# Kernel tuning notes

Hardware: AMD Instinct MI355X
Metric: run time of the kernel (lower is better)

## Reference

```python
import jax, jax.numpy as jnp
import numpy as np

D_MODEL = 1024
N_HEADS = 16
HEAD_DIM = D_MODEL // N_HEADS


def setup_inputs() -> dict:
    key = jax.random.key(0)
    k1, k2, k3, k4, k5 = jax.random.split(key, 5)
    s = 0.02
    return {
        "x": jax.random.normal(k1, (2, 2048, D_MODEL), dtype=jnp.float32),
        "w_qkv": jax.random.normal(k2, (D_MODEL, 3 * D_MODEL), dtype=jnp.float32) * s,
        "b_qkv": jax.random.normal(k3, (3 * D_MODEL,), dtype=jnp.float32) * s,
        "w_proj": jax.random.normal(k4, (D_MODEL, D_MODEL), dtype=jnp.float32) * s,
        "b_proj": jax.random.normal(k5, (D_MODEL,), dtype=jnp.float32) * s,
    }


def reference(x, w_qkv, b_qkv, w_proj, b_proj):
    B, T, C = x.shape
    # fused qkv projection: [B,T,3C] -> [3,B,H,T,Dh]
    qkv = x @ w_qkv + b_qkv
    qkv = qkv.reshape(B, T, 3, N_HEADS, HEAD_DIM).transpose(2, 0, 3, 1, 4)
    q, k, v = qkv[0], qkv[1], qkv[2]
    scale = 1.0 / np.sqrt(HEAD_DIM).astype(np.float32)
    att = jnp.einsum("bhtd,bhsd->bhts", q, k) * scale  # [B,H,T,T]
    causal = jnp.triu(jnp.ones((T, T), dtype=bool), k=1)
    att = jnp.where(causal, -jnp.inf, att)
    att = jax.nn.softmax(att, axis=-1)
    # dropout is identity in eval / p=0
    out = jnp.einsum("bhts,bhsd->bhtd", att, v)  # [B,H,T,Dh]
    out = out.transpose(0, 2, 1, 3).reshape(B, T, C)
    return out @ w_proj + b_proj
```

## Files before the change

kernel.cpp:

```cpp
#include <hip/hip_runtime.h>
#include <hip/hip_bf16.h>
#include <stdint.h>

#define MROWS 4096
#define DMODEL 1024
#define NQKV 3072
#define TSEQ 2048

typedef __attribute__((ext_vector_type(8))) short short8;
typedef __attribute__((ext_vector_type(4))) short short4v;
typedef __attribute__((ext_vector_type(4))) float floatx4;
typedef unsigned short ushort_t;

#define TILE_ELEMS 4608
#define BH_TILE_STRIDE 147456

#define QSCALE 0.1803368801111204f

static __device__ __forceinline__ unsigned short f2bf(float f) {
    union { float f; unsigned u; } v; v.f = f;
    unsigned r = v.u + 0x7fff + ((v.u >> 16) & 1);
    return (unsigned short)(r >> 16);
}


static __device__ __forceinline__ floatx4 mfma16(short4v a, short4v b, floatx4 c) {
#if defined(__HIP_DEVICE_COMPILE__)
#if __has_builtin(__builtin_amdgcn_mfma_f32_16x16x16bf16_1k)
    return __builtin_amdgcn_mfma_f32_16x16x16bf16_1k(a, b, c, 0, 0, 0);
#else
#error "mfma 16x16x16 bf16 builtin unavailable on device"
#endif
#else
    return c;
#endif
}

static __device__ __forceinline__ unsigned pk2bf(float a, float b) {
    unsigned ua = __float_as_uint(a) + 0x8000u;
    unsigned ub = __float_as_uint(b) + 0x8000u;
#if defined(__HIP_DEVICE_COMPILE__) && __has_builtin(__builtin_amdgcn_perm)
    return __builtin_amdgcn_perm(ub, ua, 0x07060302u);
#else
    return (ua >> 16) | (ub & 0xFFFF0000u);
#endif
}

static __device__ __forceinline__ unsigned cvtpk(float a, float b) {
#if defined(__HIP_DEVICE_COMPILE__)
    unsigned r;
    asm("v_cvt_pk_bf16_f32 %0, %1, %2" : "=v"(r) : "v"(a), "v"(b));
    return r;
#else
    return pk2bf(a, b);
#endif
}

static __device__ __forceinline__ float exp2_fast(float x) {
#if defined(__HIP_DEVICE_COMPILE__) && __has_builtin(__builtin_amdgcn_exp2f)
    return __builtin_amdgcn_exp2f(x);
#else
    return exp2f(x);
#endif
}

static __device__ __forceinline__ void glds16(const void* g, void* l) {
    __builtin_amdgcn_global_load_lds(
        (const __attribute__((address_space(1))) void*)g,
        (__attribute__((address_space(3))) void*)l, 16, 0, 0);
}

__global__ void cast_f32_bf16(const float* __restrict__ in,
                              ushort_t* __restrict__ out, int n) {
    int i = (blockIdx.x * blockDim.x + threadIdx.x) * 4;
    if (i < n) {
        float4 f = *(const float4*)(in + i);
        ushort4 o;
        o.x = f2bf(f.x); o.y = f2bf(f.y); o.z = f2bf(f.z); o.w = f2bf(f.w);
        *(ushort4*)(out + i) = o;
    }
}

__global__ void transpose_cast(const float* __restrict__ in,
                               ushort_t* __restrict__ out, int R, int C) {
    __shared__ float tile[32][33];
    int c0 = blockIdx.x * 32, r0 = blockIdx.y * 32;
    int tx = threadIdx.x & 31, ty = threadIdx.x >> 5;
    for (int i = 0; i < 4; i++) {
        int r = ty + i * 8;
        tile[r][tx] = in[(size_t)(r0 + r) * C + c0 + tx];
    }
    __syncthreads();
    for (int i = 0; i < 4; i++) {
        int r = ty + i * 8;
        out[(size_t)(c0 + r) * R + r0 + tx] = f2bf(tile[tx][r]);
    }
}

__global__ void transpose_v(const ushort_t* __restrict__ in,
                            ushort_t* __restrict__ out) {
    __shared__ ushort_t T[64][72];
    int tile = blockIdx.x, bh = blockIdx.y;
    int tid = threadIdx.x;
    int row = tid >> 2, q4 = tid & 3;
    const ushort_t* ip = in + ((size_t)bh * TSEQ + tile * 64) * 64;
#pragma unroll
    for (int p = 0; p < 2; p++) {
        int c = q4 * 16 + p * 8;
        *(uint4*)(&T[row][c]) = *(const uint4*)(ip + (size_t)row * 64 + c);
    }
    __syncthreads();
    ushort_t* op = out + (size_t)bh * BH_TILE_STRIDE + (size_t)tile * TILE_ELEMS;
#pragma unroll
    for (int p = 0; p < 2; p++) {
        int cbase = q4 * 16 + p * 8;
        ushort_t tmp[8];
#pragma unroll
        for (int e = 0; e < 8; e++) {
            int cp = cbase + e;
            int Q = cp >> 4, SB = (cp >> 2) & 3, J = cp & 3;
            int s = SB * 16 + Q * 4 + J;
            tmp[e] = T[s][row];
        }
        *(uint4*)(op + (size_t)row * 72 + cbase) = *(uint4*)tmp;
    }
}

template <int EPI, int MFRAG, int PERXCD>
__global__ __launch_bounds__(256, 3)
void gemm_glds(const ushort_t* __restrict__ A,
               const ushort_t* __restrict__ Bt,
               const float* __restrict__ bias,
               void* __restrict__ out0, void* __restrict__ out1, void* __restrict__ out2,
               int M, int N, int K) {
    __shared__ ushort_t As[2][MFRAG * 32 * 32];
    __shared__ ushort_t Bs[2][128 * 32];
    int tid = threadIdx.x;
    int wave = tid >> 6, lane = tid & 63;
    int quad = lane >> 4, l16 = lane & 15;
    int id = blockIdx.x;
    int xcd = id & 7, sidx = id >> 3;
    int m_idx = xcd * PERXCD + (sidx & (PERXCD - 1));
    int n_idx = sidx / PERXCD;
    int m0 = m_idx * (MFRAG * 32), n0 = n_idx * 128;
    int wm = (wave & 1) * (MFRAG * 16), wn = (wave >> 1) * 64;

    const floatx4 zero = {0.f, 0.f, 0.f, 0.f};
    floatx4 acc[MFRAG][4];
#pragma unroll
    for (int i = 0; i < MFRAG; i++)
#pragma unroll
        for (int j = 0; j < 4; j++) acc[i][j] = zero;

    int srow = tid >> 2, sc = tid & 3;
    const ushort_t* ag = A  + (size_t)(m0 + srow) * K + sc * 8;
    const ushort_t* bg = Bt + (size_t)(n0 + srow) * K + sc * 8;
    int woff = wave * 512;

    glds16(ag, &As[0][woff]);
    if (MFRAG == 4) glds16(ag + (size_t)64 * K, &As[0][woff + 2048]);
    glds16(bg, &Bs[0][woff]);
    glds16(bg + (size_t)64 * K, &Bs[0][woff + 2048]);
    __syncthreads();

    int cur = 0;
    for (int k0 = 0; k0 < K; k0 += 32) {
        if (k0 + 32 < K) {
            int nb = cur ^ 1, kn = k0 + 32;
            glds16(ag + kn, &As[nb][woff]);
            if (MFRAG == 4) glds16(ag + (size_t)64 * K + kn, &As[nb][woff + 2048]);
            glds16(bg + kn, &Bs[nb][woff]);
            glds16(bg + (size_t)64 * K + kn, &Bs[nb][woff + 2048]);
        }
        short8 af[MFRAG], bf[4];
#pragma unroll
        for (int i = 0; i < MFRAG; i++)
            af[i] = *(const short8*)(&As[cur][(wm + i * 16 + l16) * 32 + quad * 8]);
#pragma unroll
        for (int j = 0; j < 4; j++)
            bf[j] = *(const short8*)(&Bs[cur][(wn + j * 16 + l16) * 32 + quad * 8]);
#pragma unroll
        for (int i = 0; i < MFRAG; i++)
#pragma unroll
            for (int j = 0; j < 4; j++)
                acc[i][j] = __builtin_amdgcn_mfma_f32_16x16x32_bf16(
                    af[i], bf[j], acc[i][j], 0, 0, 0);
        __syncthreads();
        cur ^= 1;
    }

    int sec = n0 >> 10;
    ushort_t* dst = (ushort_t*)(sec == 0 ? out0 : (sec == 1 ? out1 : out2));

    if (EPI == 1 && sec == 2) {
#pragma unroll
        for (int i = 0; i < MFRAG; i++) {
            int row = m0 + wm + i * 16 + quad * 4;
            int Abits = ((wm >> 4) + i) & 3;
            int b = row >> 11, t = row & 2047;
            int tile = t >> 6;
            int colp = 16 * quad + 4 * Abits;
#pragma unroll
            for (int j = 0; j < 4; j++) {
                int col = n0 + wn + j * 16 + l16;
                int within = col & 1023, h = within >> 6, d = within & 63;
                size_t bh = (size_t)(b * 16 + h);
                float bvs = bias[col];
                ushort4 o;
                o.x = f2bf(acc[i][j][0] + bvs);
                o.y = f2bf(acc[i][j][1] + bvs);
                o.z = f2bf(acc[i][j][2] + bvs);
                o.w = f2bf(acc[i][j][3] + bvs);
                *(ushort4*)(dst + bh * BH_TILE_STRIDE + (size_t)tile * TILE_ELEMS
                            + (size_t)d * 72 + colp) = o;
            }
        }
        return;
    }

#pragma unroll
    for (int i = 0; i < MFRAG; i++) {
        int row = m0 + wm + i * 16 + quad * 4;
#pragma unroll
        for (int j = 0; j < 4; j++) {
            int col = n0 + wn + j * 16 + l16;
            float bvs = bias[col];
#pragma unroll
            for (int r = 0; r < 4; r++) {
                float v = acc[i][j][r] + bvs;
                int rowr = row + r;
                if (EPI == 0) {
                    ((float*)out0)[(size_t)rowr * N + col] = v;
                } else {
                    int b = rowr >> 11, t = rowr & 2047;
                    int within = col & 1023, h = within >> 6, d = within & 63;
                    size_t bh = (size_t)(b * 16 + h);
                    if (sec == 0)
                        dst[(bh * 2048 + t) * 64 + d] = f2bf(v * QSCALE);
                    else if (sec == 1)
                        dst[bh * BH_TILE_STRIDE + (size_t)(t >> 6) * TILE_ELEMS
                            + (size_t)(t & 63) * 72 + d] = f2bf(v);
                    else
                        dst[(bh * 2048 + t) * 64 + d] = f2bf(v);
                }
            }
        }
    }
}

__global__ __launch_bounds__(128, 2)
void attn_split(const ushort_t* __restrict__ Qb,
                const ushort_t* __restrict__ Kt,
                const ushort_t* __restrict__ Vt,
                ushort_t* __restrict__ outb,
                float* __restrict__ PO_a, float* __restrict__ PO_b,
                float* __restrict__ Pl_a, float* __restrict__ Pl_b) {
    __shared__ ushort_t Ks[2][64 * 72];
    __shared__ ushort_t Vs[2][64 * 72];
    int tid = threadIdx.x;
    int wave = tid >> 6, lane = tid & 63;
    int quad = lane >> 4, l16 = lane & 15;
    int id = blockIdx.x;
    int g = id >> 3;
    int bh = (id & 7) * 4 + (g >> 5);
    int rem = g & 31;
    int p = rem >> 1, sub = rem & 1;
    int b = bh >> 4, h = bh & 15;
    const ushort_t* qh = Qb + (size_t)bh * TSEQ * 64;
    const ushort_t* kh = Kt + (size_t)bh * BH_TILE_STRIDE;
    const ushort_t* vh = Vt + (size_t)bh * BH_TILE_STRIDE;
    const floatx4 zero = {0.f, 0.f, 0.f, 0.f};
    const short4v ones = {(short)0x3F80, (short)0x3F80, (short)0x3F80, (short)0x3F80};
    int lo8 = lane * 8;

    int nseg = sub ? 1 : 2;
    for (int seg = 0; seg < nseg; seg++) {
        int qt, k0, cnt, mode;
        if (sub)           { qt = 31 - p; k0 = 16 - p; cnt = 16;     mode = 2; }
        else if (seg == 0) { qt = p;      k0 = 0;      cnt = p + 1;  mode = 0; }
        else               { qt = 31 - p; k0 = 0;      cnt = 16 - p; mode = 1; }

        short8 qf0[2], qf1[2];
#pragma unroll
        for (int qs = 0; qs < 2; qs++) {
            int qrow = qt * 64 + wave * 32 + qs * 16 + l16;
            qf0[qs] = *(const short8*)(qh + (size_t)qrow * 64 + quad * 8);
            qf1[qs] = *(const short8*)(qh + (size_t)qrow * 64 + 32 + quad * 8);
        }

        floatx4 Oacc[2][4];
#pragma unroll
        for (int qs = 0; qs < 2; qs++)
#pragma unroll
            for (int j = 0; j < 4; j++) Oacc[qs][j] = zero;
        floatx4 lacc[2];
        lacc[0] = zero; lacc[1] = zero;

        __syncthreads();
        {
            const ushort_t* kt0 = kh + (size_t)k0 * TILE_ELEMS;
            const ushort_t* vt0 = vh + (size_t)k0 * TILE_ELEMS;
#pragma unroll
            for (int c = 0; c < 5; c++) {
                int cc = wave + 2 * c;
                if (cc < 9) {
                    glds16(kt0 + cc * 512 + lo8, &Ks[0][cc * 512]);
                    glds16(vt0 + cc * 512 + lo8, &Vs[0][cc * 512]);
                }
            }
        }

        for (int step = 0; step < cnt; step++) {
            int cur = step & 1;
            __syncthreads();
            if (step + 1 < cnt) {
                const ushort_t* kt = kh + (size_t)(k0 + step + 1) * TILE_ELEMS;
                const ushort_t* vt = vh + (size_t)(k0 + step + 1) * TILE_ELEMS;
#pragma unroll
                for (int c = 0; c < 5; c++) {
                    int cc = wave + 2 * c;
                    if (cc < 9) {
                        glds16(kt + cc * 512 + lo8, &Ks[cur ^ 1][cc * 512]);
                        glds16(vt + cc * 512 + lo8, &Vs[cur ^ 1][cc * 512]);
                    }
                }
            }
            const ushort_t* ks = &Ks[cur][0];
            const ushort_t* vs = &Vs[cur][0];

            floatx4 S[2][4];
            __builtin_amdgcn_s_setprio(1);
#pragma unroll
            for (int sb = 0; sb < 4; sb++) {
                short8 kf0 = *(const short8*)(ks + (sb * 16 + l16) * 72 + quad * 8);
                short8 kf1 = *(const short8*)(ks + (sb * 16 + l16) * 72 + 32 + quad * 8);
#pragma unroll
                for (int qs = 0; qs < 2; qs++) {
                    floatx4 s = zero;
                    s = __builtin_amdgcn_mfma_f32_16x16x32_bf16(kf0, qf0[qs], s, 0, 0, 0);
                    s = __builtin_amdgcn_mfma_f32_16x16x32_bf16(kf1, qf1[qs], s, 0, 0, 0);
                    S[qs][sb] = s;
                }
            }
            __builtin_amdgcn_s_setprio(0);
            if (k0 + step == qt) {
#pragma unroll
                for (int qs = 0; qs < 2; qs++) {
                    int ql = wave * 32 + qs * 16 + l16;
#pragma unroll
                    for (int sb = 0; sb < 4; sb++)
#pragma unroll
                        for (int r = 0; r < 4; r++)
                            if (sb * 16 + quad * 4 + r > ql) S[qs][sb][r] = -1e30f;
                }
            }
#pragma unroll
            for (int qs = 0; qs < 2; qs++)
#pragma unroll
                for (int sb = 0; sb < 4; sb++)
#pragma unroll
                    for (int r = 0; r < 4; r++)
                        S[qs][sb][r] = exp2_fast(S[qs][sb][r]);

            short4v pf[2][4];
#pragma unroll
            for (int qs = 0; qs < 2; qs++)
#pragma unroll
                for (int sb = 0; sb < 4; sb++) {
                    union { unsigned u[2]; short4v v; } pk;
                    pk.u[0] = cvtpk(S[qs][sb][0], S[qs][sb][1]);
                    pk.u[1] = cvtpk(S[qs][sb][2], S[qs][sb][3]);
                    pf[qs][sb] = pk.v;
                }
            __builtin_amdgcn_s_setprio(1);
#pragma unroll
            for (int qs = 0; qs < 2; qs++) {
                lacc[qs] = mfma16(ones, pf[qs][0], lacc[qs]);
                lacc[qs] = mfma16(ones, pf[qs][1], lacc[qs]);
                lacc[qs] = mfma16(ones, pf[qs][2], lacc[qs]);
                lacc[qs] = mfma16(ones, pf[qs][3], lacc[qs]);
            }
#pragma unroll
            for (int jd = 0; jd < 4; jd++) {
                const ushort_t* vrow = vs + (jd * 16 + l16) * 72 + quad * 16;
                short8 vA = *(const short8*)(vrow);
                short8 vB = *(const short8*)(vrow + 8);
                short4v v0 = __builtin_shufflevector(vA, vA, 0, 1, 2, 3);
                short4v v1 = __builtin_shufflevector(vA, vA, 4, 5, 6, 7);
                short4v v2 = __builtin_shufflevector(vB, vB, 0, 1, 2, 3);
                short4v v3 = __builtin_shufflevector(vB, vB, 4, 5, 6, 7);
#pragma unroll
                for (int qs = 0; qs < 2; qs++) {
                    Oacc[qs][jd] = mfma16(v0, pf[qs][0], Oacc[qs][jd]);
                    Oacc[qs][jd] = mfma16(v1, pf[qs][1], Oacc[qs][jd]);
                    Oacc[qs][jd] = mfma16(v2, pf[qs][2], Oacc[qs][jd]);
                    Oacc[qs][jd] = mfma16(v3, pf[qs][3], Oacc[qs][jd]);
                }
            }
            __builtin_amdgcn_s_setprio(0);
        }

        if (mode == 0) {
#pragma unroll
            for (int qs = 0; qs < 2; qs++) {
                float rl = 1.0f / lacc[qs][0];
                int row = b * TSEQ + qt * 64 + wave * 32 + qs * 16 + l16;
#pragma unroll
                for (int jd = 0; jd < 4; jd++) {
                    int col = h * 64 + jd * 16 + quad * 4;
                    ushort4 o;
                    o.x = f2bf(Oacc[qs][jd][0] * rl);
                    o.y = f2bf(Oacc[qs][jd][1] * rl);
                    o.z = f2bf(Oacc[qs][jd][2] * rl);
                    o.w = f2bf(Oacc[qs][jd][3] * rl);
                    *(ushort4*)(outb + (size_t)row * DMODEL + col) = o;
                }
            }
        } else {
            float* PO = (mode == 1) ? PO_a : PO_b;
            float* Pl = (mode == 1) ? Pl_a : Pl_b;
#pragma unroll
            for (int qs = 0; qs < 2; qs++) {
                int prow = (qt - 16) * 64 + wave * 32 + qs * 16 + l16;
                size_t rbase = ((size_t)bh * 1024 + prow) * 64;
#pragma unroll
                for (int jd = 0; jd < 4; jd++)
                    *(floatx4*)(PO + rbase + jd * 16 + quad * 4) = Oacc[qs][jd];
                if (quad == 0) Pl[(size_t)bh * 1024 + prow] = lacc[qs][0];
            }
        }
    }
}

__global__ void attn_combine(const float* __restrict__ PO_a,
                             const float* __restrict__ PO_b,
                             const float* __restrict__ Pl_a,
                             const float* __restrict__ Pl_b,
                             ushort_t* __restrict__ outb) {
    int i = blockIdx.x * 256 + threadIdx.x;
    int row = i >> 4;
    int c4 = (i & 15) * 4;
    float rl = 1.0f / (Pl_a[row] + Pl_b[row]);
    floatx4 a = *(const floatx4*)(PO_a + (size_t)row * 64 + c4);
    floatx4 c = *(const floatx4*)(PO_b + (size_t)row * 64 + c4);
    int bh = row >> 10, prow = row & 1023;
    int b = bh >> 4, h = bh & 15;
    int orow = b * TSEQ + 1024 + prow;
    ushort4 o;
    o.x = f2bf((a[0] + c[0]) * rl);
    o.y = f2bf((a[1] + c[1]) * rl);
    o.z = f2bf((a[2] + c[2]) * rl);
    o.w = f2bf((a[3] + c[3]) * rl);
    *(ushort4*)(outb + (size_t)orow * DMODEL + h * 64 + c4) = o;
}

__global__ __launch_bounds__(256, 1)
void attn_paired(const ushort_t* __restrict__ Qb,
                 const ushort_t* __restrict__ Kt,
                 const ushort_t* __restrict__ Vt,
                 ushort_t* __restrict__ outb) {
    __shared__ ushort_t Ks[2][64 * 72];
    __shared__ ushort_t Vs[2][64 * 72];
    int tid = threadIdx.x;
    int wave = tid >> 6, lane = tid & 63;
    int quad = lane >> 4, l16 = lane & 15;
    int pair = blockIdx.x;
    int bh = blockIdx.y;
    int b = bh >> 4, h = bh & 15;
    const ushort_t* qh = Qb + (size_t)bh * TSEQ * 64;
    const ushort_t* kh = Kt + (size_t)bh * BH_TILE_STRIDE;
    const ushort_t* vh = Vt + (size_t)bh * BH_TILE_STRIDE;
    const floatx4 zero = {0.f, 0.f, 0.f, 0.f};
    int lo8 = lane * 8;

    for (int half = 0; half < 2; half++) {
        int qt = half ? (31 - pair) : pair;
        int q0 = qt * 64;
        int nsteps = qt + 1;

        int qrow = q0 + wave * 16 + l16;
        short8 qf0 = *(const short8*)(qh + (size_t)qrow * 64 + quad * 8);
        short8 qf1 = *(const short8*)(qh + (size_t)qrow * 64 + 32 + quad * 8);

        floatx4 Oacc[4];
#pragma unroll
        for (int j = 0; j < 4; j++) Oacc[j] = zero;
        float lsum = 0.f;

#pragma unroll
        for (int c = 0; c < 3; c++) {
            int cc = wave + 4 * c;
            if (cc < 9) {
                glds16(kh + cc * 512 + lo8, &Ks[0][cc * 512]);
                glds16(vh + cc * 512 + lo8, &Vs[0][cc * 512]);
            }
        }

        for (int step = 0; step < nsteps; step++) {
            int cur = step & 1;
            __syncthreads();
            if (step + 1 < nsteps) {
                const ushort_t* kt = kh + (size_t)(step + 1) * TILE_ELEMS;
                const ushort_t* vt = vh + (size_t)(step + 1) * TILE_ELEMS;
#pragma unroll
                for (int c = 0; c < 3; c++) {
                    int cc = wave + 4 * c;
                    if (cc < 9) {
                        glds16(kt + cc * 512 + lo8, &Ks[cur ^ 1][cc * 512]);
                        glds16(vt + cc * 512 + lo8, &Vs[cur ^ 1][cc * 512]);
                    }
                }
            }
            const ushort_t* ks = &Ks[cur][0];
            const ushort_t* vs = &Vs[cur][0];

            floatx4 S[4];
#pragma unroll
            for (int sb = 0; sb < 4; sb++) {
                short8 kf0 = *(const short8*)(ks + (sb * 16 + l16) * 72 + quad * 8);
                short8 kf1 = *(const short8*)(ks + (sb * 16 + l16) * 72 + 32 + quad * 8);
                floatx4 s = zero;
                s = __builtin_amdgcn_mfma_f32_16x16x32_bf16(kf0, qf0, s, 0, 0, 0);
                s = __builtin_amdgcn_mfma_f32_16x16x32_bf16(kf1, qf1, s, 0, 0, 0);
                S[sb] = s;
            }
            if (step == nsteps - 1) {
                int ql = wave * 16 + l16;
#pragma unroll
                for (int sb = 0; sb < 4; sb++)
#pragma unroll
                    for (int r = 0; r < 4; r++)
                        if (sb * 16 + quad * 4 + r > ql) S[sb][r] = -1e30f;
            }
            float sum = 0.f;
#pragma unroll
            for (int sb = 0; sb < 4; sb++)
#pragma unroll
                for (int r = 0; r < 4; r++) {
                    float p = exp2_fast(S[sb][r]);
                    S[sb][r] = p;
                    sum += p;
                }
            lsum += sum;

            short4v pf[4];
#pragma unroll
            for (int sb = 0; sb < 4; sb++) {
                union { unsigned u[2]; short4v v; } pk;
                pk.u[0] = pk2bf(S[sb][0], S[sb][1]);
                pk.u[1] = pk2bf(S[sb][2], S[sb][3]);
                pf[sb] = pk.v;
            }
#pragma unroll
            for (int jd = 0; jd < 4; jd++) {
                const ushort_t* vrow = vs + (jd * 16 + l16) * 72 + quad * 16;
                short8 vA = *(const short8*)(vrow);
                short8 vB = *(const short8*)(vrow + 8);
                short4v v0 = __builtin_shufflevector(vA, vA, 0, 1, 2, 3);
                short4v v1 = __builtin_shufflevector(vA, vA, 4, 5, 6, 7);
                short4v v2 = __builtin_shufflevector(vB, vB, 0, 1, 2, 3);
                short4v v3 = __builtin_shufflevector(vB, vB, 4, 5, 6, 7);
                Oacc[jd] = mfma16(v0, pf[0], Oacc[jd]);
                Oacc[jd] = mfma16(v1, pf[1], Oacc[jd]);
                Oacc[jd] = mfma16(v2, pf[2], Oacc[jd]);
                Oacc[jd] = mfma16(v3, pf[3], Oacc[jd]);
            }
        }
        {
            float l = lsum;
            l += __shfl_xor(l, 16);
            l += __shfl_xor(l, 32);
            float rl = 1.0f / l;
            int row = b * TSEQ + q0 + wave * 16 + l16;
#pragma unroll
            for (int jd = 0; jd < 4; jd++) {
                int col = h * 64 + jd * 16 + quad * 4;
                ushort4 o;
                o.x = f2bf(Oacc[jd][0] * rl);
                o.y = f2bf(Oacc[jd][1] * rl);
                o.z = f2bf(Oacc[jd][2] * rl);
                o.w = f2bf(Oacc[jd][3] * rl);
                *(ushort4*)(outb + (size_t)row * DMODEL + col) = o;
            }
        }
        __syncthreads();
    }
}

extern "C" void kernel_launch(void* const* d_in, const int* in_sizes, int n_in,
                              void* d_out, int out_size, void* d_ws, size_t ws_size,
                              hipStream_t stream) {
    const float* x      = (const float*)d_in[0];
    const float* w_qkv  = (const float*)d_in[1];
    const float* b_qkv  = (const float*)d_in[2];
    const float* w_proj = (const float*)d_in[3];
    const float* b_proj = (const float*)d_in[4];
    float* out = (float*)d_out;
    char* ws = (char*)d_ws;

    ushort_t* xb     = (ushort_t*)(ws);
    ushort_t* wqkvT  = (ushort_t*)(ws + 8388608);
    ushort_t* wprojT = (ushort_t*)(ws + 10485760);
    ushort_t* Qb     = (ushort_t*)(ws + 14680064);
    ushort_t* Kt     = (ushort_t*)(ws + 23068672);
    ushort_t* attnb  = (ushort_t*)(ws + 32505856);
    ushort_t* Vt     = (ushort_t*)(ws + 40894464);
    float* PO_a = (float*)(ws + 50331648);
    float* PO_b = (float*)(ws + 58720256);
    float* Pl_a = (float*)(ws + 67108864);
    float* Pl_b = (float*)(ws + 67239936);
    const size_t ws_need = 67371008;

    cast_f32_bf16<<<4096, 256, 0, stream>>>(x, xb, MROWS * DMODEL);
    transpose_cast<<<dim3(NQKV / 32, DMODEL / 32), 256, 0, stream>>>(w_qkv, wqkvT, DMODEL, NQKV);

    if (ws_size >= ws_need) {
        gemm_glds<1, 4, 4><<<768, 256, 0, stream>>>(
            xb, wqkvT, b_qkv, Qb, Kt, Vt, MROWS, NQKV, DMODEL);
        transpose_cast<<<dim3(DMODEL / 32, DMODEL / 32), 256, 0, stream>>>(w_proj, wprojT, DMODEL, DMODEL);
        attn_split<<<dim3(1024), 128, 0, stream>>>(Qb, Kt, Vt, attnb,
                                                   PO_a, PO_b, Pl_a, Pl_b);
        attn_combine<<<dim3(2048), 256, 0, stream>>>(PO_a, PO_b, Pl_a, Pl_b, attnb);
    } else {
        ushort_t* Vb    = (ushort_t*)(ws + 32505856);
        ushort_t* VtOld = (ushort_t*)(ws);
        gemm_glds<2, 4, 4><<<768, 256, 0, stream>>>(
            xb, wqkvT, b_qkv, Qb, Kt, Vb, MROWS, NQKV, DMODEL);
        transpose_v<<<dim3(32, 32), 256, 0, stream>>>(Vb, VtOld);
        transpose_cast<<<dim3(DMODEL / 32, DMODEL / 32), 256, 0, stream>>>(w_proj, wprojT, DMODEL, DMODEL);
        attn_paired<<<dim3(16, 32), 256, 0, stream>>>(Qb, Kt, VtOld, Vb);
    }

    gemm_glds<0, 2, 8><<<512, 256, 0, stream>>>(
        attnb, wprojT, b_proj, out, nullptr, nullptr, MROWS, DMODEL, DMODEL);
}
```

Measured before the change: 180.7 us.

## Pre-swizzle GEMM operands in global memory to avoid LDS bank conflicts

Producers of the GEMM operands (activation cast, weight transpose-casts, attention output writers) now write each row's 8-element groups XOR-permuted by the row index. The GEMM reads LDS fragments with the matching XOR, so the direct global-to-LDS copies keep their linear layout while the fragment reads spread across LDS banks. This is meant to remove bank conflicts on the LDS fragment loads without extra shuffle work in the GEMM. It adds index arithmetic, and every producer and consumer must agree on the layout. The fallback path keeps the old layout for the projection input.

New measurement: 183.7 us. Within noise of the previous version (+1.7%).

```diff
diff --git a/kernel.cpp b/kernel.cpp
--- a/kernel.cpp
+++ b/kernel.cpp
@@ -77,12 +77,13 @@
         float4 f = *(const float4*)(in + i);
         ushort4 o;
         o.x = f2bf(f.x); o.y = f2bf(f.y); o.z = f2bf(f.z); o.w = f2bf(f.w);
-        *(ushort4*)(out + i) = o;
+        int oi = i ^ (((i >> 10) & 3) << 3);
+        *(ushort4*)(out + oi) = o;
     }
 }
 
 __global__ void transpose_cast(const float* __restrict__ in,
-                               ushort_t* __restrict__ out, int R, int C) {
+                               ushort_t* __restrict__ out, int R, int C, int swz) {
     __shared__ float tile[32][33];
     int c0 = blockIdx.x * 32, r0 = blockIdx.y * 32;
     int tx = threadIdx.x & 31, ty = threadIdx.x >> 5;
@@ -93,7 +94,10 @@
     __syncthreads();
     for (int i = 0; i < 4; i++) {
         int r = ty + i * 8;
-        out[(size_t)(c0 + r) * R + r0 + tx] = f2bf(tile[tx][r]);
+        int orow = c0 + r;
+        int k = r0 + tx;
+        int kk = swz ? (k ^ ((orow & 3) << 3)) : k;
+        out[(size_t)orow * R + kk] = f2bf(tile[tx][r]);
     }
 }
 
@@ -126,7 +130,7 @@
     }
 }
 
-template <int EPI, int MFRAG, int PERXCD>
+template <int EPI, int MFRAG, int PERXCD, int SWZ>
 __global__ __launch_bounds__(256, 3)
 void gemm_glds(const ushort_t* __restrict__ A,
                const ushort_t* __restrict__ Bt,
@@ -174,11 +178,17 @@
         }
         short8 af[MFRAG], bf[4];
 #pragma unroll
-        for (int i = 0; i < MFRAG; i++)
-            af[i] = *(const short8*)(&As[cur][(wm + i * 16 + l16) * 32 + quad * 8]);
-#pragma unroll
-        for (int j = 0; j < 4; j++)
-            bf[j] = *(const short8*)(&Bs[cur][(wn + j * 16 + l16) * 32 + quad * 8]);
+        for (int i = 0; i < MFRAG; i++) {
+            int ar = wm + i * 16 + l16;
+            int idx = (ar * 32 + quad * 8) ^ (SWZ ? ((ar & 3) << 3) : 0);
+            af[i] = *(const short8*)(&As[cur][idx]);
+        }
+#pragma unroll
+        for (int j = 0; j < 4; j++) {
+            int br = wn + j * 16 + l16;
+            int idx = (br * 32 + quad * 8) ^ (SWZ ? ((br & 3) << 3) : 0);
+            bf[j] = *(const short8*)(&Bs[cur][idx]);
+        }
 #pragma unroll
         for (int i = 0; i < MFRAG; i++)
 #pragma unroll
@@ -408,12 +418,13 @@
 #pragma unroll
                 for (int jd = 0; jd < 4; jd++) {
                     int col = h * 64 + jd * 16 + quad * 4;
+                    int colS = col ^ ((row & 3) << 3);
                     ushort4 o;
                     o.x = f2bf(Oacc[qs][jd][0] * rl);
                     o.y = f2bf(Oacc[qs][jd][1] * rl);
                     o.z = f2bf(Oacc[qs][jd][2] * rl);
                     o.w = f2bf(Oacc[qs][jd][3] * rl);
-                    *(ushort4*)(outb + (size_t)row * DMODEL + col) = o;
+                    *(ushort4*)(outb + (size_t)row * DMODEL + colS) = o;
                 }
             }
         } else {
@@ -446,12 +457,14 @@
     int bh = row >> 10, prow = row & 1023;
     int b = bh >> 4, h = bh & 15;
     int orow = b * TSEQ + 1024 + prow;
+    int col = h * 64 + c4;
+    int colS = col ^ ((orow & 3) << 3);
     ushort4 o;
     o.x = f2bf((a[0] + c[0]) * rl);
     o.y = f2bf((a[1] + c[1]) * rl);
     o.z = f2bf((a[2] + c[2]) * rl);
     o.w = f2bf((a[3] + c[3]) * rl);
-    *(ushort4*)(outb + (size_t)orow * DMODEL + h * 64 + c4) = o;
+    *(ushort4*)(outb + (size_t)orow * DMODEL + colS) = o;
 }
 
 __global__ __launch_bounds__(256, 1)
@@ -612,25 +625,26 @@
     const size_t ws_need = 67371008;
 
     cast_f32_bf16<<<4096, 256, 0, stream>>>(x, xb, MROWS * DMODEL);
-    transpose_cast<<<dim3(NQKV / 32, DMODEL / 32), 256, 0, stream>>>(w_qkv, wqkvT, DMODEL, NQKV);
+    transpose_cast<<<dim3(NQKV / 32, DMODEL / 32), 256, 0, stream>>>(w_qkv, wqkvT, DMODEL, NQKV, 1);
 
     if (ws_size >= ws_need) {
-        gemm_glds<1, 4, 4><<<768, 256, 0, stream>>>(
+        gemm_glds<1, 4, 4, 1><<<768, 256, 0, stream>>>(
             xb, wqkvT, b_qkv, Qb, Kt, Vt, MROWS, NQKV, DMODEL);
-        transpose_cast<<<dim3(DMODEL / 32, DMODEL / 32), 256, 0, stream>>>(w_proj, wprojT, DMODEL, DMODEL);
+        transpose_cast<<<dim3(DMODEL / 32, DMODEL / 32), 256, 0, stream>>>(w_proj, wprojT, DMODEL, DMODEL, 1);
         attn_split<<<dim3(1024), 128, 0, stream>>>(Qb, Kt, Vt, attnb,
                                                    PO_a, PO_b, Pl_a, Pl_b);
         attn_combine<<<dim3(2048), 256, 0, stream>>>(PO_a, PO_b, Pl_a, Pl_b, attnb);
+        gemm_glds<0, 2, 8, 1><<<512, 256, 0, stream>>>(
+            attnb, wprojT, b_proj, out, nullptr, nullptr, MROWS, DMODEL, DMODEL);
     } else {
         ushort_t* Vb    = (ushort_t*)(ws + 32505856);
         ushort_t* VtOld = (ushort_t*)(ws);
-        gemm_glds<2, 4, 4><<<768, 256, 0, stream>>>(
+        gemm_glds<2, 4, 4, 1><<<768, 256, 0, stream>>>(
             xb, wqkvT, b_qkv, Qb, Kt, Vb, MROWS, NQKV, DMODEL);
         transpose_v<<<dim3(32, 32), 256, 0, stream>>>(Vb, VtOld);
-        transpose_cast<<<dim3(DMODEL / 32, DMODEL / 32), 256, 0, stream>>>(w_proj, wprojT, DMODEL, DMODEL);
+        transpose_cast<<<dim3(DMODEL / 32, DMODEL / 32), 256, 0, stream>>>(w_proj, wprojT, DMODEL, DMODEL, 0);
         attn_paired<<<dim3(16, 32), 256, 0, stream>>>(Qb, Kt, VtOld, Vb);
-    }
-
-    gemm_glds<0, 2, 8><<<512, 256, 0, stream>>>(
-        attnb, wprojT, b_proj, out, nullptr, nullptr, MROWS, DMODEL, DMODEL);
-}
+        gemm_glds<0, 2, 8, 0><<<512, 256, 0, stream>>>(
+            Vb, wprojT, b_proj, out, nullptr, nullptr, MROWS, DMODEL, DMODEL);
+    }
+}
```

## Triple-buffer GEMM LDS tiles with explicit vmcnt waits instead of syncthreads

Applied to the files above, without the earlier changes.

The bf16 GEMM moves from double to triple LDS buffering, prefetching two k-steps ahead. It uses explicit s_waitcnt vmcnt counts plus raw s_barrier in place of __syncthreads, so later global-to-LDS loads stay in flight while the current tile is consumed. This is meant to hide global load latency that the old full drain at every step exposed. It costs 50% more LDS per block, which may cut occupancy under the launch bounds, and correctness depends on the hand-computed wait counts. The fallback path also now runs the projection GEMM on the buffer that attn_paired writes.

After: 184.5 us. 2.1% more time.

```diff
diff --git a/kernel.cpp b/kernel.cpp
--- a/kernel.cpp
+++ b/kernel.cpp
@@ -70,6 +70,22 @@
         (__attribute__((address_space(3))) void*)l, 16, 0, 0);
 }
 
+template <int N>
+static __device__ __forceinline__ void waitcnt_vm() {
+#if defined(__HIP_DEVICE_COMPILE__)
+    if constexpr (N == 8)      asm volatile("s_waitcnt vmcnt(8)" ::: "memory");
+    else if constexpr (N == 6) asm volatile("s_waitcnt vmcnt(6)" ::: "memory");
+    else if constexpr (N == 4) asm volatile("s_waitcnt vmcnt(4)" ::: "memory");
+    else if constexpr (N == 3) asm volatile("s_waitcnt vmcnt(3)" ::: "memory");
+    else                       asm volatile("s_waitcnt vmcnt(0)" ::: "memory");
+#endif
+}
+static __device__ __forceinline__ void waitcnt_lgkm0() {
+#if defined(__HIP_DEVICE_COMPILE__)
+    asm volatile("s_waitcnt lgkmcnt(0)" ::: "memory");
+#endif
+}
+
 __global__ void cast_f32_bf16(const float* __restrict__ in,
                               ushort_t* __restrict__ out, int n) {
     int i = (blockIdx.x * blockDim.x + threadIdx.x) * 4;
@@ -133,8 +149,9 @@
                const float* __restrict__ bias,
                void* __restrict__ out0, void* __restrict__ out1, void* __restrict__ out2,
                int M, int N, int K) {
-    __shared__ ushort_t As[2][MFRAG * 32 * 32];
-    __shared__ ushort_t Bs[2][128 * 32];
+    __shared__ ushort_t As[3][MFRAG * 32 * 32];
+    __shared__ ushort_t Bs[3][128 * 32];
+    constexpr int L = (MFRAG == 4) ? 4 : 3;
     int tid = threadIdx.x;
     int wave = tid >> 6, lane = tid & 63;
     int quad = lane >> 4, l16 = lane & 15;
@@ -157,37 +174,48 @@
     const ushort_t* bg = Bt + (size_t)(n0 + srow) * K + sc * 8;
     int woff = wave * 512;
 
-    glds16(ag, &As[0][woff]);
-    if (MFRAG == 4) glds16(ag + (size_t)64 * K, &As[0][woff + 2048]);
-    glds16(bg, &Bs[0][woff]);
-    glds16(bg + (size_t)64 * K, &Bs[0][woff + 2048]);
-    __syncthreads();
+#define STAGE(kofs, buf)                                                    \
+    do {                                                                    \
+        glds16(ag + (kofs), &As[buf][woff]);                                \
+        if (MFRAG == 4) glds16(ag + (size_t)64 * K + (kofs), &As[buf][woff + 2048]); \
+        glds16(bg + (kofs), &Bs[buf][woff]);                                \
+        glds16(bg + (size_t)64 * K + (kofs), &Bs[buf][woff + 2048]);        \
+    } while (0)
+
+    int nsteps = K >> 5;
+    STAGE(0, 0);
+    STAGE(32, 1);
+    __builtin_amdgcn_s_barrier();
 
     int cur = 0;
-    for (int k0 = 0; k0 < K; k0 += 32) {
-        if (k0 + 32 < K) {
-            int nb = cur ^ 1, kn = k0 + 32;
-            glds16(ag + kn, &As[nb][woff]);
-            if (MFRAG == 4) glds16(ag + (size_t)64 * K + kn, &As[nb][woff + 2048]);
-            glds16(bg + kn, &Bs[nb][woff]);
-            glds16(bg + (size_t)64 * K + kn, &Bs[nb][woff + 2048]);
+    for (int i = 0; i < nsteps; i++) {
+        if (i + 2 < nsteps) {
+            int pb = (cur == 0) ? 2 : cur - 1;
+            STAGE((i + 2) << 5, pb);
+            waitcnt_vm<2 * L>();
+        } else if (i + 1 < nsteps) {
+            waitcnt_vm<L>();
+        } else {
+            waitcnt_vm<0>();
         }
         short8 af[MFRAG], bf[4];
 #pragma unroll
-        for (int i = 0; i < MFRAG; i++)
-            af[i] = *(const short8*)(&As[cur][(wm + i * 16 + l16) * 32 + quad * 8]);
+        for (int j = 0; j < MFRAG; j++)
+            af[j] = *(const short8*)(&As[cur][(wm + j * 16 + l16) * 32 + quad * 8]);
 #pragma unroll
         for (int j = 0; j < 4; j++)
             bf[j] = *(const short8*)(&Bs[cur][(wn + j * 16 + l16) * 32 + quad * 8]);
 #pragma unroll
-        for (int i = 0; i < MFRAG; i++)
-#pragma unroll
-            for (int j = 0; j < 4; j++)
-                acc[i][j] = __builtin_amdgcn_mfma_f32_16x16x32_bf16(
-                    af[i], bf[j], acc[i][j], 0, 0, 0);
-        __syncthreads();
-        cur ^= 1;
-    }
+        for (int j = 0; j < MFRAG; j++)
+#pragma unroll
+            for (int k = 0; k < 4; k++)
+                acc[j][k] = __builtin_amdgcn_mfma_f32_16x16x32_bf16(
+                    af[j], bf[k], acc[j][k], 0, 0, 0);
+        waitcnt_lgkm0();
+        __builtin_amdgcn_s_barrier();
+        cur = (cur == 2) ? 0 : cur + 1;
+    }
+#undef STAGE
 
     int sec = n0 >> 10;
     ushort_t* dst = (ushort_t*)(sec == 0 ? out0 : (sec == 1 ? out1 : out2));
@@ -629,6 +657,9 @@
         transpose_v<<<dim3(32, 32), 256, 0, stream>>>(Vb, VtOld);
         transpose_cast<<<dim3(DMODEL / 32, DMODEL / 32), 256, 0, stream>>>(w_proj, wprojT, DMODEL, DMODEL);
         attn_paired<<<dim3(16, 32), 256, 0, stream>>>(Qb, Kt, VtOld, Vb);
+        gemm_glds<0, 2, 8><<<512, 256, 0, stream>>>(
+            Vb, wprojT, b_proj, out, nullptr, nullptr, MROWS, DMODEL, DMODEL);
+        return;
     }
 
     gemm_glds<0, 2, 8><<<512, 256, 0, stream>>>(
```

## Process both sub=0 query tiles in one pass sharing K/V tile loads

Applied to the files above, without the earlier changes.

In the split attention kernel, blocks with sub==0 previously ran two sequential segments (query tile p, then query tile 31-p), each streaming the same leading K/V tiles from key tile 0. Now both query tiles run in a single loop over max(limA,limB)+1 key tiles, sharing each K/V load and the LDS fragment reads, with per-tile predicates gating the MFMA work. This cuts redundant global-to-LDS traffic and barriers, at the cost of more registers for two sets of Q fragments and accumulators, which can lower occupancy. The fallback path also gains an explicit projection GEMM call and return.

Result: slower. 184.8 us (+2.3%).

```diff
diff --git a/kernel.cpp b/kernel.cpp
--- a/kernel.cpp
+++ b/kernel.cpp
@@ -273,12 +273,200 @@
     const short4v ones = {(short)0x3F80, (short)0x3F80, (short)0x3F80, (short)0x3F80};
     int lo8 = lane * 8;
 
-    int nseg = sub ? 1 : 2;
-    for (int seg = 0; seg < nseg; seg++) {
-        int qt, k0, cnt, mode;
-        if (sub)           { qt = 31 - p; k0 = 16 - p; cnt = 16;     mode = 2; }
-        else if (seg == 0) { qt = p;      k0 = 0;      cnt = p + 1;  mode = 0; }
-        else               { qt = 31 - p; k0 = 0;      cnt = 16 - p; mode = 1; }
+    if (sub == 0) {
+        int qtA = p, qtB = 31 - p;
+        int limA = p, limB = 15 - p;
+        int cnt = (limA > limB ? limA : limB) + 1;
+
+        short8 qAf0[2], qAf1[2], qBf0[2], qBf1[2];
+#pragma unroll
+        for (int qs = 0; qs < 2; qs++) {
+            int rA = qtA * 64 + wave * 32 + qs * 16 + l16;
+            int rB = qtB * 64 + wave * 32 + qs * 16 + l16;
+            qAf0[qs] = *(const short8*)(qh + (size_t)rA * 64 + quad * 8);
+            qAf1[qs] = *(const short8*)(qh + (size_t)rA * 64 + 32 + quad * 8);
+            qBf0[qs] = *(const short8*)(qh + (size_t)rB * 64 + quad * 8);
+            qBf1[qs] = *(const short8*)(qh + (size_t)rB * 64 + 32 + quad * 8);
+        }
+
+        floatx4 OA[2][4], OB[2][4], lA[2], lB[2];
+#pragma unroll
+        for (int qs = 0; qs < 2; qs++) {
+            lA[qs] = zero; lB[qs] = zero;
+#pragma unroll
+            for (int j = 0; j < 4; j++) { OA[qs][j] = zero; OB[qs][j] = zero; }
+        }
+
+#pragma unroll
+        for (int c = 0; c < 5; c++) {
+            int cc = wave + 2 * c;
+            if (cc < 9) {
+                glds16(kh + cc * 512 + lo8, &Ks[0][cc * 512]);
+                glds16(vh + cc * 512 + lo8, &Vs[0][cc * 512]);
+            }
+        }
+
+        for (int s = 0; s < cnt; s++) {
+            int cur = s & 1;
+            __syncthreads();
+            if (s + 1 < cnt) {
+                const ushort_t* kt = kh + (size_t)(s + 1) * TILE_ELEMS;
+                const ushort_t* vt = vh + (size_t)(s + 1) * TILE_ELEMS;
+#pragma unroll
+                for (int c = 0; c < 5; c++) {
+                    int cc = wave + 2 * c;
+                    if (cc < 9) {
+                        glds16(kt + cc * 512 + lo8, &Ks[cur ^ 1][cc * 512]);
+                        glds16(vt + cc * 512 + lo8, &Vs[cur ^ 1][cc * 512]);
+                    }
+                }
+            }
+            const ushort_t* ks = &Ks[cur][0];
+            const ushort_t* vs = &Vs[cur][0];
+            bool doA = (s <= limA), doB = (s <= limB);
+
+            short4v pfA[2][4], pfB[2][4];
+            if (doA) {
+                floatx4 SA[2][4];
+                __builtin_amdgcn_s_setprio(1);
+#pragma unroll
+                for (int sb = 0; sb < 4; sb++) {
+                    short8 kf0 = *(const short8*)(ks + (sb * 16 + l16) * 72 + quad * 8);
+                    short8 kf1 = *(const short8*)(ks + (sb * 16 + l16) * 72 + 32 + quad * 8);
+#pragma unroll
+                    for (int qs = 0; qs < 2; qs++) {
+                        floatx4 t = zero;
+                        t = __builtin_amdgcn_mfma_f32_16x16x32_bf16(kf0, qAf0[qs], t, 0, 0, 0);
+                        t = __builtin_amdgcn_mfma_f32_16x16x32_bf16(kf1, qAf1[qs], t, 0, 0, 0);
+                        SA[qs][sb] = t;
+                    }
+                }
+                __builtin_amdgcn_s_setprio(0);
+                if (s == limA) {
+#pragma unroll
+                    for (int qs = 0; qs < 2; qs++) {
+                        int ql = wave * 32 + qs * 16 + l16;
+#pragma unroll
+                        for (int sb = 0; sb < 4; sb++)
+#pragma unroll
+                            for (int r = 0; r < 4; r++)
+                                if (sb * 16 + quad * 4 + r > ql) SA[qs][sb][r] = -1e30f;
+                    }
+                }
+#pragma unroll
+                for (int qs = 0; qs < 2; qs++)
+#pragma unroll
+                    for (int sb = 0; sb < 4; sb++) {
+#pragma unroll
+                        for (int r = 0; r < 4; r++) SA[qs][sb][r] = exp2_fast(SA[qs][sb][r]);
+                        union { unsigned u[2]; short4v v; } pk;
+                        pk.u[0] = cvtpk(SA[qs][sb][0], SA[qs][sb][1]);
+                        pk.u[1] = cvtpk(SA[qs][sb][2], SA[qs][sb][3]);
+                        pfA[qs][sb] = pk.v;
+                    }
+            }
+            if (doB) {
+                floatx4 SB[2][4];
+                __builtin_amdgcn_s_setprio(1);
+#pragma unroll
+                for (int sb = 0; sb < 4; sb++) {
+                    short8 kf0 = *(const short8*)(ks + (sb * 16 + l16) * 72 + quad * 8);
+                    short8 kf1 = *(const short8*)(ks + (sb * 16 + l16) * 72 + 32 + quad * 8);
+#pragma unroll
+                    for (int qs = 0; qs < 2; qs++) {
+                        floatx4 t = zero;
+                        t = __builtin_amdgcn_mfma_f32_16x16x32_bf16(kf0, qBf0[qs], t, 0, 0, 0);
+                        t = __builtin_amdgcn_mfma_f32_16x16x32_bf16(kf1, qBf1[qs], t, 0, 0, 0);
+                        SB[qs][sb] = t;
+                    }
+                }
+                __builtin_amdgcn_s_setprio(0);
+#pragma unroll
+                for (int qs = 0; qs < 2; qs++)
+#pragma unroll
+                    for (int sb = 0; sb < 4; sb++) {
+#pragma unroll
+                        for (int r = 0; r < 4; r++) SB[qs][sb][r] = exp2_fast(SB[qs][sb][r]);
+                        union { unsigned u[2]; short4v v; } pk;
+                        pk.u[0] = cvtpk(SB[qs][sb][0], SB[qs][sb][1]);
+                        pk.u[1] = cvtpk(SB[qs][sb][2], SB[qs][sb][3]);
+                        pfB[qs][sb] = pk.v;
+                    }
+            }
+
+            __builtin_amdgcn_s_setprio(1);
+#pragma unroll
+            for (int qs = 0; qs < 2; qs++) {
+                if (doA) {
+                    lA[qs] = mfma16(ones, pfA[qs][0], lA[qs]);
+                    lA[qs] = mfma16(ones, pfA[qs][1], lA[qs]);
+                    lA[qs] = mfma16(ones, pfA[qs][2], lA[qs]);
+                    lA[qs] = mfma16(ones, pfA[qs][3], lA[qs]);
+                }
+                if (doB) {
+                    lB[qs] = mfma16(ones, pfB[qs][0], lB[qs]);
+                    lB[qs] = mfma16(ones, pfB[qs][1], lB[qs]);
+                    lB[qs] = mfma16(ones, pfB[qs][2], lB[qs]);
+                    lB[qs] = mfma16(ones, pfB[qs][3], lB[qs]);
+                }
+            }
+#pragma unroll
+            for (int jd = 0; jd < 4; jd++) {
+                const ushort_t* vrow = vs + (jd * 16 + l16) * 72 + quad * 16;
+                short8 vA8 = *(const short8*)(vrow);
+                short8 vB8 = *(const short8*)(vrow + 8);
+                short4v v0 = __builtin_shufflevector(vA8, vA8, 0, 1, 2, 3);
+                short4v v1 = __builtin_shufflevector(vA8, vA8, 4, 5, 6, 7);
+                short4v v2 = __builtin_shufflevector(vB8, vB8, 0, 1, 2, 3);
+                short4v v3 = __builtin_shufflevector(vB8, vB8, 4, 5, 6, 7);
+#pragma unroll
+                for (int qs = 0; qs < 2; qs++) {
+                    if (doA) {
+                        OA[qs][jd] = mfma16(v0, pfA[qs][0], OA[qs][jd]);
+                        OA[qs][jd] = mfma16(v1, pfA[qs][1], OA[qs][jd]);
+                        OA[qs][jd] = mfma16(v2, pfA[qs][2], OA[qs][jd]);
+                        OA[qs][jd] = mfma16(v3, pfA[qs][3], OA[qs][jd]);
+                    }
+                    if (doB) {
+                        OB[qs][jd] = mfma16(v0, pfB[qs][0], OB[qs][jd]);
+                        OB[qs][jd] = mfma16(v1, pfB[qs][1], OB[qs][jd]);
+                        OB[qs][jd] = mfma16(v2, pfB[qs][2], OB[qs][jd]);
+                        OB[qs][jd] = mfma16(v3, pfB[qs][3], OB[qs][jd]);
+                    }
+                }
+            }
+            __builtin_amdgcn_s_setprio(0);
+        }
+
+#pragma unroll
+        for (int qs = 0; qs < 2; qs++) {
+            float rl = 1.0f / lA[qs][0];
+            int row = b * TSEQ + qtA * 64 + wave * 32 + qs * 16 + l16;
+#pragma unroll
+            for (int jd = 0; jd < 4; jd++) {
+                int col = h * 64 + jd * 16 + quad * 4;
+                ushort4 o;
+                o.x = f2bf(OA[qs][jd][0] * rl);
+                o.y = f2bf(OA[qs][jd][1] * rl);
+                o.z = f2bf(OA[qs][jd][2] * rl);
+                o.w = f2bf(OA[qs][jd][3] * rl);
+                *(ushort4*)(outb + (size_t)row * DMODEL + col) = o;
+            }
+        }
+#pragma unroll
+        for (int qs = 0; qs < 2; qs++) {
+            int prow = (qtB - 16) * 64 + wave * 32 + qs * 16 + l16;
+            size_t rbase = ((size_t)bh * 1024 + prow) * 64;
+#pragma unroll
+            for (int jd = 0; jd < 4; jd++)
+                *(floatx4*)(PO_a + rbase + jd * 16 + quad * 4) = OB[qs][jd];
+            if (quad == 0) Pl_a[(size_t)bh * 1024 + prow] = lB[qs][0];
+        }
+        return;
+    }
+
+    {
+        int qt = 31 - p, k0 = 16 - p, cnt = 16;
 
         short8 qf0[2], qf1[2];
 #pragma unroll
@@ -296,7 +484,6 @@
         floatx4 lacc[2];
         lacc[0] = zero; lacc[1] = zero;
 
-        __syncthreads();
         {
             const ushort_t* kt0 = kh + (size_t)k0 * TILE_ELEMS;
             const ushort_t* vt0 = vh + (size_t)k0 * TILE_ELEMS;
@@ -336,10 +523,10 @@
                 short8 kf1 = *(const short8*)(ks + (sb * 16 + l16) * 72 + 32 + quad * 8);
 #pragma unroll
                 for (int qs = 0; qs < 2; qs++) {
-                    floatx4 s = zero;
-                    s = __builtin_amdgcn_mfma_f32_16x16x32_bf16(kf0, qf0[qs], s, 0, 0, 0);
-                    s = __builtin_amdgcn_mfma_f32_16x16x32_bf16(kf1, qf1[qs], s, 0, 0, 0);
-                    S[qs][sb] = s;
+                    floatx4 t = zero;
+                    t = __builtin_amdgcn_mfma_f32_16x16x32_bf16(kf0, qf0[qs], t, 0, 0, 0);
+                    t = __builtin_amdgcn_mfma_f32_16x16x32_bf16(kf1, qf1[qs], t, 0, 0, 0);
+                    S[qs][sb] = t;
                 }
             }
             __builtin_amdgcn_s_setprio(0);
@@ -383,12 +570,12 @@
 #pragma unroll
             for (int jd = 0; jd < 4; jd++) {
                 const ushort_t* vrow = vs + (jd * 16 + l16) * 72 + quad * 16;
-                short8 vA = *(const short8*)(vrow);
-                short8 vB = *(const short8*)(vrow + 8);
-                short4v v0 = __builtin_shufflevector(vA, vA, 0, 1, 2, 3);
-                short4v v1 = __builtin_shufflevector(vA, vA, 4, 5, 6, 7);
-                short4v v2 = __builtin_shufflevector(vB, vB, 0, 1, 2, 3);
-                short4v v3 = __builtin_shufflevector(vB, vB, 4, 5, 6, 7);
+                short8 vA8 = *(const short8*)(vrow);
+                short8 vB8 = *(const short8*)(vrow + 8);
+                short4v v0 = __builtin_shufflevector(vA8, vA8, 0, 1, 2, 3);
+                short4v v1 = __builtin_shufflevector(vA8, vA8, 4, 5, 6, 7);
+                short4v v2 = __builtin_shufflevector(vB8, vB8, 0, 1, 2, 3);
+                short4v v3 = __builtin_shufflevector(vB8, vB8, 4, 5, 6, 7);
 #pragma unroll
                 for (int qs = 0; qs < 2; qs++) {
                     Oacc[qs][jd] = mfma16(v0, pf[qs][0], Oacc[qs][jd]);
@@ -400,34 +587,14 @@
             __builtin_amdgcn_s_setprio(0);
         }
 
-        if (mode == 0) {
-#pragma unroll
-            for (int qs = 0; qs < 2; qs++) {
-                float rl = 1.0f / lacc[qs][0];
-                int row = b * TSEQ + qt * 64 + wave * 32 + qs * 16 + l16;
-#pragma unroll
-                for (int jd = 0; jd < 4; jd++) {
-                    int col = h * 64 + jd * 16 + quad * 4;
-                    ushort4 o;
-                    o.x = f2bf(Oacc[qs][jd][0] * rl);
-                    o.y = f2bf(Oacc[qs][jd][1] * rl);
-                    o.z = f2bf(Oacc[qs][jd][2] * rl);
-                    o.w = f2bf(Oacc[qs][jd][3] * rl);
-                    *(ushort4*)(outb + (size_t)row * DMODEL + col) = o;
-                }
-            }
-        } else {
-            float* PO = (mode == 1) ? PO_a : PO_b;
-            float* Pl = (mode == 1) ? Pl_a : Pl_b;
-#pragma unroll
-            for (int qs = 0; qs < 2; qs++) {
-                int prow = (qt - 16) * 64 + wave * 32 + qs * 16 + l16;
-                size_t rbase = ((size_t)bh * 1024 + prow) * 64;
-#pragma unroll
-                for (int jd = 0; jd < 4; jd++)
-                    *(floatx4*)(PO + rbase + jd * 16 + quad * 4) = Oacc[qs][jd];
-                if (quad == 0) Pl[(size_t)bh * 1024 + prow] = lacc[qs][0];
-            }
+#pragma unroll
+        for (int qs = 0; qs < 2; qs++) {
+            int prow = (qt - 16) * 64 + wave * 32 + qs * 16 + l16;
+            size_t rbase = ((size_t)bh * 1024 + prow) * 64;
+#pragma unroll
+            for (int jd = 0; jd < 4; jd++)
+                *(floatx4*)(PO_b + rbase + jd * 16 + quad * 4) = Oacc[qs][jd];
+            if (quad == 0) Pl_b[(size_t)bh * 1024 + prow] = lacc[qs][0];
         }
     }
 }
@@ -629,6 +796,9 @@
         transpose_v<<<dim3(32, 32), 256, 0, stream>>>(Vb, VtOld);
         transpose_cast<<<dim3(DMODEL / 32, DMODEL / 32), 256, 0, stream>>>(w_proj, wprojT, DMODEL, DMODEL);
         attn_paired<<<dim3(16, 32), 256, 0, stream>>>(Qb, Kt, VtOld, Vb);
+        gemm_glds<0, 2, 8><<<512, 256, 0, stream>>>(
+            Vb, wprojT, b_proj, out, nullptr, nullptr, MROWS, DMODEL, DMODEL);
+        return;
     }
 
     gemm_glds<0, 2, 8><<<512, 256, 0, stream>>>(
```
